# Kernel optimization log

Hardware: AMD Instinct MI355X
Metric: run time of the kernel (lower is better)

The kernel has to match this reference:

```python
import jax, jax.numpy as jnp
import numpy as np


def _top2_margin(logits, targets):
    # logits: [N, C], targets: [N] int
    top2, _ = jax.lax.top_k(logits, 2)                       # [N, 2]
    tgt_logit = jnp.take_along_axis(logits, targets[:, None], axis=1)[:, 0]  # [N]
    # margin = top1 - top2 if the target class attains the max, else 0
    return jnp.where(tgt_logit == top2[:, 0], top2[:, 0] - top2[:, 1],
                     jnp.zeros((), dtype=logits.dtype))


def setup_inputs() -> dict:
    key = jax.random.key(0)
    ks = jax.random.split(key, 6)
    N, C = 16384, 1000
    return {
        "outputs1": jax.random.normal(ks[0], (N, C), dtype=jnp.float32),
        "outputs2": jax.random.normal(ks[1], (N, C), dtype=jnp.float32),
        "outputs3": jax.random.normal(ks[2], (N, C), dtype=jnp.float32),
        "outputs4": jax.random.normal(ks[3], (N, C), dtype=jnp.float32),
        "mimic": jax.random.normal(ks[4], (N, C), dtype=jnp.float32),
        "targets": jax.random.randint(ks[5], (N,), 0, C, dtype=jnp.int64),
        "n_test": N,
    }


def reference(outputs1, outputs2, outputs3, outputs4, mimic, targets, n_test):
    T = 2.0  # temperature (init kwarg)
    # n_test == N; the loop over samples is fully vectorized here.
    margins = jnp.stack([
        _top2_margin(outputs1, targets),
        _top2_margin(outputs2, targets),
        _top2_margin(outputs3, targets),
        _top2_margin(outputs4, targets),
        _top2_margin(mimic, targets),
    ], axis=1)                                               # [N, 5]
    out_threshold = jax.nn.softmax(margins / T, axis=1)      # [N, 5]
    max_preds = jnp.maximum(jnp.maximum(outputs1.max(), outputs2.max()),
                            jnp.maximum(outputs3.max(), outputs4.max()))
    return (max_preds, out_threshold)
```

## Files before the change

kernel.cpp:

```cpp
#include <hip/hip_runtime.h>
#include <math.h>

#define NROWS 16384
#define NCOLS 1000
#define NMAT  5
#define WPB   4
#define BLOCKS_A (NROWS / WPB)

__global__ __launch_bounds__(256) void fused_kernel(
    const float* __restrict__ o0, const float* __restrict__ o1,
    const float* __restrict__ o2, const float* __restrict__ o3,
    const float* __restrict__ o4, const int* __restrict__ targets,
    float* __restrict__ out, float* __restrict__ blockmax)
{
    const int wave = threadIdx.x >> 6;
    const int lane = threadIdx.x & 63;
    const int row  = blockIdx.x * WPB + wave;

    const float* rows[NMAT];
    rows[0] = o0 + (size_t)row * NCOLS;
    rows[1] = o1 + (size_t)row * NCOLS;
    rows[2] = o2 + (size_t)row * NCOLS;
    rows[3] = o3 + (size_t)row * NCOLS;
    rows[4] = o4 + (size_t)row * NCOLS;

    float4 v[NMAT][4];
    #pragma unroll
    for (int m = 0; m < NMAT; ++m) {
        const float4* b = (const float4*)rows[m];
        v[m][0] = b[lane];
        v[m][1] = b[lane + 64];
        v[m][2] = b[lane + 128];
        v[m][3] = make_float4(-INFINITY, -INFINITY, -INFINITY, -INFINITY);
    }
    if (lane < 58) {
        #pragma unroll
        for (int m = 0; m < NMAT; ++m)
            v[m][3] = ((const float4*)rows[m])[lane + 192];
    }

    float t1[NMAT], t2[NMAT];
#define UPD(m, x) { float _mn = fminf(t1[m], (x)); t1[m] = fmaxf(t1[m], (x)); \
                    t2[m] = fmaxf(t2[m], _mn); }
    #pragma unroll
    for (int m = 0; m < NMAT; ++m) {
        t1[m] = -INFINITY; t2[m] = -INFINITY;
        #pragma unroll
        for (int q = 0; q < 4; ++q) {
            UPD(m, v[m][q].x) UPD(m, v[m][q].y)
            UPD(m, v[m][q].z) UPD(m, v[m][q].w)
        }
    }
#undef UPD

    #pragma unroll
    for (int off = 32; off > 0; off >>= 1) {
        float a1[NMAT], a2[NMAT];
        #pragma unroll
        for (int m = 0; m < NMAT; ++m) {
            a1[m] = __shfl_xor(t1[m], off);
            a2[m] = __shfl_xor(t2[m], off);
        }
        #pragma unroll
        for (int m = 0; m < NMAT; ++m) {
            float mn = fminf(t1[m], a1[m]);
            t1[m] = fmaxf(t1[m], a1[m]);
            t2[m] = fmaxf(fmaxf(t2[m], a2[m]), mn);
        }
    }

    if (lane == 0) {
        const int t = targets[row];
        float mg[NMAT];
        #pragma unroll
        for (int m = 0; m < NMAT; ++m) {
            const float tgt = rows[m][t];
            mg[m] = (tgt == t1[m]) ? (t1[m] - t2[m]) : 0.0f;
        }
        float mx = mg[0];
        #pragma unroll
        for (int m = 1; m < NMAT; ++m) mx = fmaxf(mx, mg[m]);
        float e[NMAT], s = 0.0f;
        #pragma unroll
        for (int m = 0; m < NMAT; ++m) { e[m] = __expf((mg[m] - mx) * 0.5f); s += e[m]; }
        const float inv = 1.0f / s;
        #pragma unroll
        for (int m = 0; m < NMAT; ++m) out[1 + row * NMAT + m] = e[m] * inv;
    }

    __shared__ float smax[WPB];
    if (lane == 0)
        smax[wave] = fmaxf(fmaxf(t1[0], t1[1]), fmaxf(t1[2], t1[3]));
    __syncthreads();
    if (threadIdx.x == 0)
        blockmax[blockIdx.x] =
            fmaxf(fmaxf(smax[0], smax[1]), fmaxf(smax[2], smax[3]));
}

__global__ __launch_bounds__(256) void reduce_kernel(
    const float* __restrict__ blockmax, float* __restrict__ out)
{
    __shared__ float red[256];
    float mm = -INFINITY;
    for (int k = threadIdx.x; k < BLOCKS_A; k += 256)
        mm = fmaxf(mm, blockmax[k]);
    red[threadIdx.x] = mm;
    __syncthreads();
    #pragma unroll
    for (int s = 128; s > 0; s >>= 1) {
        if (threadIdx.x < s)
            red[threadIdx.x] = fmaxf(red[threadIdx.x], red[threadIdx.x + s]);
        __syncthreads();
    }
    if (threadIdx.x == 0) out[0] = red[0];
}

extern "C" void kernel_launch(void* const* d_in, const int* in_sizes, int n_in,
                              void* d_out, int out_size, void* d_ws, size_t ws_size,
                              hipStream_t stream) {
    const float* o0 = (const float*)d_in[0];
    const float* o1 = (const float*)d_in[1];
    const float* o2 = (const float*)d_in[2];
    const float* o3 = (const float*)d_in[3];
    const float* o4 = (const float*)d_in[4];
    const int*   tg = (const int*)d_in[5];
    float* out = (float*)d_out;

    float* blockmax = (float*)d_ws;

    fused_kernel<<<BLOCKS_A, 256, 0, stream>>>(o0, o1, o2, o3, o4, tg,
                                               out, blockmax);
    reduce_kernel<<<1, 256, 0, stream>>>(blockmax, out);
}
```

Measured before the change: 293.6 us.

## Double-buffer rows via global_load_lds with one wave processing many rows

Replaces the one-row-per-wave register load scheme with single-wave blocks that each process sixteen rows. Rows are streamed into two LDS buffers using direct global-to-LDS loads, with manual vmcnt waits so the next row's fetch overlaps the current row's reduction. The target logit is read from LDS instead of a second global load, and the softmax outputs are written by five lanes in parallel. This aims to keep more memory requests in flight per wave, at the cost of fewer blocks, higher LDS use per block and hand-tuned waitcnt logic that depends on the exact number of issued loads.

```diff
diff --git a/kernel.cpp b/kernel.cpp
--- a/kernel.cpp
+++ b/kernel.cpp
@@ -1,108 +1,132 @@
 #include <hip/hip_runtime.h>
 #include <math.h>
+#include <stdint.h>
 
 #define NROWS 16384
 #define NCOLS 1000
 #define NMAT  5
-#define WPB   4
-#define BLOCKS_A (NROWS / WPB)
+#define RPB   16
+#define NBLK  (NROWS / RPB)
+#define NINF  (-INFINITY)
 
-__global__ __launch_bounds__(256) void fused_kernel(
+__device__ __forceinline__ void gld16(const float4* g, float4* l) {
+    __builtin_amdgcn_global_load_lds(
+        (const __attribute__((address_space(1))) void*)(uintptr_t)g,
+        (__attribute__((address_space(3))) void*)(uint32_t)(uintptr_t)l,
+        16, 0, 0);
+}
+
+#define PREFETCH(row, buf) do {                                               \
+    _Pragma("unroll")                                                         \
+    for (int _m = 0; _m < NMAT; ++_m) {                                       \
+        const float4* _g = (const float4*)(mats[_m] + (size_t)(row) * NCOLS); \
+        _Pragma("unroll")                                                     \
+        for (int _s = 0; _s < 3; ++_s)                                        \
+            gld16(_g + _s * 64 + lane, &buf[_m][_s * 64]);                    \
+    }                                                                         \
+    if (lane < 58) {                                                          \
+        _Pragma("unroll")                                                     \
+        for (int _m = 0; _m < NMAT; ++_m) {                                   \
+            const float4* _g = (const float4*)(mats[_m] + (size_t)(row) * NCOLS); \
+            gld16(_g + 192 + lane, &buf[_m][192]);                            \
+        }                                                                     \
+    }                                                                         \
+} while (0)
+
+#define UPD(m, x) { float _mn = fminf(t1[m], (x)); t1[m] = fmaxf(t1[m], (x)); \
+                    t2[m] = fmaxf(t2[m], _mn); }
+
+#define PROCESS(buf, row) do {                                                \
+    const int _t = targets[row];                                              \
+    float t1[NMAT], t2[NMAT];                                                 \
+    _Pragma("unroll")                                                         \
+    for (int _m = 0; _m < NMAT; ++_m) {                                       \
+        t1[_m] = NINF; t2[_m] = NINF;                                         \
+        _Pragma("unroll")                                                     \
+        for (int _s = 0; _s < 4; ++_s) {                                      \
+            float4 _x = buf[_m][_s * 64 + lane];                              \
+            if (_s == 3 && lane >= 58) {                                      \
+                _x.x = NINF; _x.y = NINF; _x.z = NINF; _x.w = NINF;           \
+            }                                                                 \
+            UPD(_m, _x.x) UPD(_m, _x.y) UPD(_m, _x.z) UPD(_m, _x.w)          \
+        }                                                                     \
+    }                                                                         \
+    _Pragma("unroll")                                                         \
+    for (int _off = 32; _off > 0; _off >>= 1) {                               \
+        float _a1[NMAT], _a2[NMAT];                                           \
+        _Pragma("unroll")                                                     \
+        for (int _m = 0; _m < NMAT; ++_m) {                                   \
+            _a1[_m] = __shfl_xor(t1[_m], _off);                               \
+            _a2[_m] = __shfl_xor(t2[_m], _off);                               \
+        }                                                                     \
+        _Pragma("unroll")                                                     \
+        for (int _m = 0; _m < NMAT; ++_m) {                                   \
+            float _mn = fminf(t1[_m], _a1[_m]);                               \
+            t1[_m] = fmaxf(t1[_m], _a1[_m]);                                  \
+            t2[_m] = fmaxf(fmaxf(t2[_m], _a2[_m]), _mn);                      \
+        }                                                                     \
+    }                                                                         \
+    const float* _bf = (const float*)&buf[0][0];                              \
+    float _mg[NMAT];                                                          \
+    _Pragma("unroll")                                                         \
+    for (int _m = 0; _m < NMAT; ++_m) {                                       \
+        const float _tg = _bf[_m * 1024 + _t];        \
+        _mg[_m] = (_tg == t1[_m]) ? (t1[_m] - t2[_m]) : 0.0f;                 \
+    }                                                                         \
+    float _mx = _mg[0];                                                       \
+    _Pragma("unroll")                                                         \
+    for (int _m = 1; _m < NMAT; ++_m) _mx = fmaxf(_mx, _mg[_m]);              \
+    float _e[NMAT], _ss = 0.0f;                                               \
+    _Pragma("unroll")                                                         \
+    for (int _m = 0; _m < NMAT; ++_m) {                                       \
+        _e[_m] = __expf((_mg[_m] - _mx) * 0.5f); _ss += _e[_m];               \
+    }                                                                         \
+    const float _inv = 1.0f / _ss;                                            \
+    float _wv = _e[0] * _inv;                                                 \
+    if (lane == 1) _wv = _e[1] * _inv;                                        \
+    if (lane == 2) _wv = _e[2] * _inv;                                        \
+    if (lane == 3) _wv = _e[3] * _inv;                                        \
+    if (lane == 4) _wv = _e[4] * _inv;                                        \
+    if (lane < NMAT) out[1 + (size_t)(row) * NMAT + lane] = _wv;              \
+    bmax = fmaxf(bmax, fmaxf(fmaxf(t1[0], t1[1]), fmaxf(t1[2], t1[3])));      \
+} while (0)
+
+__global__ __launch_bounds__(64) void fused_kernel(
     const float* __restrict__ o0, const float* __restrict__ o1,
     const float* __restrict__ o2, const float* __restrict__ o3,
     const float* __restrict__ o4, const int* __restrict__ targets,
     float* __restrict__ out, float* __restrict__ blockmax)
 {
-    const int wave = threadIdx.x >> 6;
-    const int lane = threadIdx.x & 63;
-    const int row  = blockIdx.x * WPB + wave;
+    const int lane = threadIdx.x;
+    const int row0 = blockIdx.x * RPB;
 
-    const float* rows[NMAT];
-    rows[0] = o0 + (size_t)row * NCOLS;
-    rows[1] = o1 + (size_t)row * NCOLS;
-    rows[2] = o2 + (size_t)row * NCOLS;
-    rows[3] = o3 + (size_t)row * NCOLS;
-    rows[4] = o4 + (size_t)row * NCOLS;
+    __shared__ float4 bufA[NMAT][256];
+    __shared__ float4 bufB[NMAT][256];
+    const float* mats[NMAT] = {o0, o1, o2, o3, o4};
+    float bmax = NINF;
 
-    float4 v[NMAT][4];
-    #pragma unroll
-    for (int m = 0; m < NMAT; ++m) {
-        const float4* b = (const float4*)rows[m];
-        v[m][0] = b[lane];
-        v[m][1] = b[lane + 64];
-        v[m][2] = b[lane + 128];
-        v[m][3] = make_float4(-INFINITY, -INFINITY, -INFINITY, -INFINITY);
+    PREFETCH(row0, bufA);
+    for (int i = 0; i < RPB; i += 2) {
+        PREFETCH(row0 + i + 1, bufB);
+        asm volatile("s_waitcnt vmcnt(20)" ::: "memory");
+        PROCESS(bufA, row0 + i);
+        if (i + 2 < RPB) {
+            PREFETCH(row0 + i + 2, bufA);
+            asm volatile("s_waitcnt vmcnt(20)" ::: "memory");
+        } else {
+            asm volatile("s_waitcnt vmcnt(0)" ::: "memory");
+        }
+        PROCESS(bufB, row0 + i + 1);
     }
-    if (lane < 58) {
-        #pragma unroll
-        for (int m = 0; m < NMAT; ++m)
-            v[m][3] = ((const float4*)rows[m])[lane + 192];
-    }
-
-    float t1[NMAT], t2[NMAT];
-#define UPD(m, x) { float _mn = fminf(t1[m], (x)); t1[m] = fmaxf(t1[m], (x)); \
-                    t2[m] = fmaxf(t2[m], _mn); }
-    #pragma unroll
-    for (int m = 0; m < NMAT; ++m) {
-        t1[m] = -INFINITY; t2[m] = -INFINITY;
-        #pragma unroll
-        for (int q = 0; q < 4; ++q) {
-            UPD(m, v[m][q].x) UPD(m, v[m][q].y)
-            UPD(m, v[m][q].z) UPD(m, v[m][q].w)
-        }
-    }
-#undef UPD
-
-    #pragma unroll
-    for (int off = 32; off > 0; off >>= 1) {
-        float a1[NMAT], a2[NMAT];
-        #pragma unroll
-        for (int m = 0; m < NMAT; ++m) {
-            a1[m] = __shfl_xor(t1[m], off);
-            a2[m] = __shfl_xor(t2[m], off);
-        }
-        #pragma unroll
-        for (int m = 0; m < NMAT; ++m) {
-            float mn = fminf(t1[m], a1[m]);
-            t1[m] = fmaxf(t1[m], a1[m]);
-            t2[m] = fmaxf(fmaxf(t2[m], a2[m]), mn);
-        }
-    }
-
-    if (lane == 0) {
-        const int t = targets[row];
-        float mg[NMAT];
-        #pragma unroll
-        for (int m = 0; m < NMAT; ++m) {
-            const float tgt = rows[m][t];
-            mg[m] = (tgt == t1[m]) ? (t1[m] - t2[m]) : 0.0f;
-        }
-        float mx = mg[0];
-        #pragma unroll
-        for (int m = 1; m < NMAT; ++m) mx = fmaxf(mx, mg[m]);
-        float e[NMAT], s = 0.0f;
-        #pragma unroll
-        for (int m = 0; m < NMAT; ++m) { e[m] = __expf((mg[m] - mx) * 0.5f); s += e[m]; }
-        const float inv = 1.0f / s;
-        #pragma unroll
-        for (int m = 0; m < NMAT; ++m) out[1 + row * NMAT + m] = e[m] * inv;
-    }
-
-    __shared__ float smax[WPB];
-    if (lane == 0)
-        smax[wave] = fmaxf(fmaxf(t1[0], t1[1]), fmaxf(t1[2], t1[3]));
-    __syncthreads();
-    if (threadIdx.x == 0)
-        blockmax[blockIdx.x] =
-            fmaxf(fmaxf(smax[0], smax[1]), fmaxf(smax[2], smax[3]));
+    if (lane == 0) blockmax[blockIdx.x] = bmax;
 }
 
 __global__ __launch_bounds__(256) void reduce_kernel(
     const float* __restrict__ blockmax, float* __restrict__ out)
 {
     __shared__ float red[256];
-    float mm = -INFINITY;
-    for (int k = threadIdx.x; k < BLOCKS_A; k += 256)
+    float mm = NINF;
+    for (int k = threadIdx.x; k < NBLK; k += 256)
         mm = fmaxf(mm, blockmax[k]);
     red[threadIdx.x] = mm;
     __syncthreads();
@@ -128,7 +152,7 @@
 
     float* blockmax = (float*)d_ws;
 
-    fused_kernel<<<BLOCKS_A, 256, 0, stream>>>(o0, o1, o2, o3, o4, tg,
-                                               out, blockmax);
+    fused_kernel<<<NBLK, 64, 0, stream>>>(o0, o1, o2, o3, o4, tg,
+                                          out, blockmax);
     reduce_kernel<<<1, 256, 0, stream>>>(blockmax, out);
 }
```

After: 307.0 us. 1.05x slower.
